# Performance work log

Measured on AMD Instinct MI355X. Metric: run time of the kernel, lower is better.

## Reference

```python
import jax, jax.numpy as jnp
import numpy as np

HR, LR, K, RANK = 2048, 1024, 8, 16


def setup_inputs() -> dict:
    key = jax.random.key(0)
    kA, kX, kW, kU, kV, kM = jax.random.split(key, 6)
    A = jax.random.normal(kA, (LR, LR), dtype=jnp.float32)
    A = (A + A.T) / 2  # symmetric so torch UPLO='U' and jax eigh agree
    X = jax.random.normal(kX, (LR, HR), dtype=jnp.float32)
    init_range = (6.0 / (HR + HR)) ** 0.5  # glorot uniform
    weights = jax.random.uniform(kW, (HR, HR), dtype=jnp.float32,
                                 minval=-init_range, maxval=init_range)
    Us = jax.random.normal(kU, (K, HR, RANK), dtype=jnp.float32) * 0.001
    # original inits Vs to zeros; use small noise so corrections are nonzero
    Vs = jax.random.normal(kV, (K, HR, RANK), dtype=jnp.float32) * 0.01
    alphas = jnp.ones((K,), dtype=jnp.float32) / K
    masks = (jax.random.uniform(kM, (K, HR, HR)) < 0.5).astype(jnp.float32)
    return {"A": A, "X": X, "weights": weights, "Us": Us, "Vs": Vs,
            "alphas": alphas, "masks": masks}


def _set_unit_diag(M, eye):
    return M * (1.0 - eye) + eye


def reference(A, X, weights, Us, Vs, alphas, masks):
    lr = A.shape[0]
    hr = weights.shape[0]
    eye_hr = jnp.eye(hr, dtype=A.dtype)
    # --- GSRLayer ---
    _, U_lr = jnp.linalg.eigh(A)                      # (lr, lr)
    s_d = jnp.concatenate([jnp.eye(lr, dtype=A.dtype),
                           jnp.eye(lr, dtype=A.dtype)], axis=0)  # (hr, lr)
    f_d = weights @ s_d @ U_lr.T @ X                  # (hr, hr)
    adj = jnp.abs(f_d)
    adj = _set_unit_diag(adj, eye_hr)
    # --- community-aware low-rank corrections ---
    alpha = jax.nn.softmax(alphas)                    # (k,)
    Zm = adj[None, :, :] * masks                      # (k, hr, hr)
    t = jnp.einsum('kij,kjr->kir', Zm, Us)            # (k, hr, rank)
    corr = jnp.einsum('kir,kjr->kij', t, Vs) * masks  # (k, hr, hr)
    out_adj = adj + jnp.einsum('k,kij->ij', alpha, corr)
    # --- symmetrize with unit diagonal ---
    X_out = out_adj @ out_adj.T
    X_out = (X_out + X_out.T) / 2
    X_out = _set_unit_diag(X_out, eye_hr)
    return out_adj, jnp.abs(X_out)
```

## Files before the change

### kernel.cpp

```cpp
#include <hip/hip_runtime.h>
#include <hip/hip_bf16.h>

typedef unsigned long long u64;

#define MBYTE (1ull << 20)

static const size_t OFF_A64   = 0;
static const size_t OFF_VT    = 8*MBYTE;
static const size_t OFF_TAU   = 12*MBYTE;
static const size_t OFF_D64   = 12*MBYTE +  8192;
static const size_t OFF_E64   = 12*MBYTE + 16384;
static const size_t OFF_XB    = 12*MBYTE + 24576;
static const size_t OFF_Y2B   = 12*MBYTE + 32768;
static const size_t OFF_Y1B   = 12*MBYTE + 40960;
static const size_t OFF_XA    = 12*MBYTE + 49152;
static const size_t OFF_Y1A   = 12*MBYTE + 57344;
static const size_t OFF_Y2A   = 12*MBYTE + 65536;
static const size_t OFF_QA    = 13*MBYTE;
static const size_t OFF_QB    = 17*MBYTE;
static const size_t OFF_SHAT  = 21*MBYTE;
static const size_t OFF_WC    = 25*MBYTE;
static const size_t OFF_M1    = 33*MBYTE;
static const size_t OFF_T8    = 33*MBYTE;
static const size_t OFF_ALPHA = 35*MBYTE + 512*1024;
static const size_t OFF_ADJ   = 41*MBYTE;
static const size_t OFF_OADJ  = 17*MBYTE;
static const size_t OFF_CBUF  = 0;

static const size_t SCD_STRIDE = 9216;
static const size_t SCI_STRIDE = 6144;
static const size_t OFF_SCDB  = OFF_WC;
static const size_t OFF_SCIB  = OFF_WC + 2359296;
static const size_t OFF_KNB   = OFF_WC + 2359296 + 786432;
static const size_t OFF_KNDB  = OFF_WC + 2359296 + 786432 + 2048;

static const size_t OFF_WYW   = OFF_WC;
static const size_t OFF_WYTW  = OFF_WC + 524288;
static const size_t OFF_WYG   = OFF_WC + 1048576;


__global__ void kCopyA(const float* __restrict__ A, double* __restrict__ A64) {
  int gid = blockIdx.x*256 + threadIdx.x;
  if (gid < 1024*1024) A64[gid] = (double)A[gid];
}

__device__ __forceinline__ double agLoadD(const double* p) {
  return __hip_atomic_load(p, __ATOMIC_RELAXED, __HIP_MEMORY_SCOPE_AGENT);
}
__device__ __forceinline__ void agStoreD(double* p, double v) {
  __hip_atomic_store(p, v, __ATOMIC_RELAXED, __HIP_MEMORY_SCOPE_AGENT);
}

#define TD_NBLK 64

__global__ __launch_bounds__(1024) void kTriDiag(
    double* __restrict__ A64,
    double* __restrict__ y1A, double* __restrict__ y1B,
    double* __restrict__ y2A, double* __restrict__ y2B,
    double* __restrict__ diagP, unsigned* __restrict__ flags,
    double* __restrict__ tauv, double* __restrict__ e64, double* __restrict__ d64,
    float* __restrict__ Vt) {
  __shared__ double xL[1024], vL[1024], wL[1024], y1L[1024], y2L[1024];
  __shared__ double red[4];
  __shared__ double sS[4];
  int tid = threadIdx.x;
  int bid = blockIdx.x;
  bool w0 = (bid == 0);
  int lane = tid & 63, wave = tid >> 6;
  int myRow = wave*TD_NBLK + bid;

  double dg = 0.0;

  for (int i = 0; i <= 1023; ++i) {
    const double* y1in = (((i-1)&1) != 0) ? y1B : y1A;
    const double* y2in = (((i-1)&1) != 0) ? y2B : y2A;
    double* y1out = ((i&1) != 0) ? y1B : y1A;
    double* y2out = ((i&1) != 0) ? y2B : y2A;

    if (i == 0) {
      if (tid < 256) {
        for (int c = tid; c < 1024; c += 256) { vL[c] = 0.0; wL[c] = 0.0; }
        for (int c = 1 + tid; c < 1024; c += 256) xL[c] = A64[(u64)c*1024];
        if (w0 && tid == 0) d64[0] = A64[0];
      }
      __syncthreads();
    } else {
      int j = i - 1;
      double sy1 = agLoadD(&y1in[tid]);
      double sy2 = agLoadD(&y2in[tid]);
      if (w0 && tid == 0) dg = agLoadD(&diagP[i]);
      double acc = 0.0;
      if (tid < 256) {
        for (int c = i + 1 + tid; c < 1024; c += 256) { double v = xL[c]; acc += v*v; }
        for (int off = 32; off > 0; off >>= 1) acc += __shfl_xor(acc, off, 64);
      }
      y1L[tid] = sy1; y2L[tid] = sy2;
      if (tid < 256 && lane == 0) red[wave] = acc;
      __syncthreads();
      if (tid == 0) {
        double xn2 = red[0] + red[1] + red[2] + red[3];
        double alpha = xL[i];
        double tv, sc;
        if (xn2 == 0.0) { tv = 0.0; if (w0) e64[j] = alpha; sc = 0.0; }
        else {
          double beta = (alpha >= 0.0) ? -sqrt(alpha*alpha + xn2) : sqrt(alpha*alpha + xn2);
          tv = (beta - alpha)/beta;
          if (w0) e64[j] = beta;
          sc = 1.0/(alpha - beta);
        }
        if (w0) tauv[j] = tv;
        sS[0] = sc; sS[1] = tv;
        vL[i] = 1.0;
        if (w0) Vt[(u64)j*1024 + i] = 1.0f;
      }
      __syncthreads();
      if (tid < 256) {
        double sc = sS[0], tv = sS[1];
        double acc2 = 0.0;
        for (int r = i + tid; r < 1024; r += 256) {
          double v;
          if (r == i) v = 1.0;
          else {
            v = xL[r]*sc;
            vL[r] = v;
            if (w0) Vt[(u64)j*1024 + r] = (float)v;
          }
          double P = tv*(y1L[r] + sc*y2L[r]);
          wL[r] = P;
          acc2 += P*v;
        }
        for (int off = 32; off > 0; off >>= 1) acc2 += __shfl_xor(acc2, off, 64);
        if (lane == 0) red[wave] = acc2;
      }
      __syncthreads();
      if (tid == 0) {
        double coef = 0.5*sS[1]*(red[0] + red[1] + red[2] + red[3]);
        double wi = wL[i] - coef;
        sS[2] = coef; sS[3] = wi;
        if (w0) d64[i] = dg - 2.0*wi;
      }
      __syncthreads();
      if (tid < 256) {
        double coef = sS[2], wi = sS[3];
        for (int r = i + tid; r < 1024; r += 256) {
          double wcr = wL[r] - coef*vL[r];
          wL[r] = wcr;
          if (r > i) xL[r] = y1L[r] - vL[r]*wi - wcr;
        }
      }
      __syncthreads();
    }
    if (i <= 1022) {
      int r = myRow;
      if (r >= i + 1) {
        double vr = vL[r], wr = wL[r];
        double* Arow = A64 + (u64)r*1024;
        double acc = 0.0, y1v = 0.0;
        for (int c = i + 1 + lane; c < 1024; c += 64) {
          double a = Arow[c] - vr*wL[c] - wr*vL[c];
          Arow[c] = a;
          if (c == r) agStoreD(&diagP[r], a);
          if (c == i + 1) y1v = a; else acc += a*xL[c];
        }
        for (int off = 32; off > 0; off >>= 1) acc += __shfl_down(acc, off, 64);
        if (lane == 0) { agStoreD(&y1out[r], y1v); agStoreD(&y2out[r], acc); }
      }
      __syncthreads();
      unsigned tgt = (unsigned)(i + 1);
      if (tid == 0)
        __hip_atomic_store(&flags[bid*16], tgt, __ATOMIC_RELEASE, __HIP_MEMORY_SCOPE_AGENT);
      if (tid < TD_NBLK) {
        for (;;) {
          unsigned v = __hip_atomic_load(&flags[tid*16], __ATOMIC_ACQUIRE, __HIP_MEMORY_SCOPE_AGENT);
          if (__all(v >= tgt)) break;
          __builtin_amdgcn_s_sleep(2);
        }
      }
      __syncthreads();
    }
  }
  if (w0 && tid == 0) {
    for (int c = 16; c < 1024; c += 16) {
      double ae = fabs(e64[c-1]);
      d64[c-1] -= ae;
      d64[c]   -= ae;
    }
  }
}


__device__ void slartg_(double f, double g, double* cs, double* sn, double* r) {
  if (g == 0.0) { *cs = 1.0; *sn = 0.0; *r = f; }
  else if (f == 0.0) { *cs = 0.0; *sn = (g >= 0.0) ? 1.0 : -1.0; *r = fabs(g); }
  else {
    double d = sqrt(f*f + g*g);
    *cs = fabs(f)/d;
    *r = (f >= 0.0) ? d : -d;
    *sn = g / (*r);
  }
}

__device__ void slaev2_(double a, double b, double c, double* rt1, double* rt2,
                        double* cs1, double* sn1) {
  double sm = a + c, df = a - c, adf = fabs(df), tb = b + b, ab = fabs(tb);
  double acmx, acmn;
  if (fabs(a) > fabs(c)) { acmx = a; acmn = c; } else { acmx = c; acmn = a; }
  double rt;
  if (adf > ab) rt = adf*sqrt(1.0 + (ab/adf)*(ab/adf));
  else if (adf < ab) rt = ab*sqrt(1.0 + (adf/ab)*(adf/ab));
  else rt = ab*sqrt(2.0);
  int sgn1;
  if (sm < 0.0) { *rt1 = 0.5*(sm - rt); sgn1 = -1; *rt2 = (acmx / *rt1)*acmn - (b / *rt1)*b; }
  else if (sm > 0.0) { *rt1 = 0.5*(sm + rt); sgn1 = 1; *rt2 = (acmx / *rt1)*acmn - (b / *rt1)*b; }
  else { *rt1 = 0.5*rt; *rt2 = -0.5*rt; sgn1 = 1; }
  int sgn2; double cs;
  if (df >= 0.0) { cs = df + rt; sgn2 = 1; } else { cs = df - rt; sgn2 = -1; }
  double acs = fabs(cs);
  if (acs > ab) { double ct = -tb/cs; *sn1 = 1.0/sqrt(1.0 + ct*ct); *cs1 = ct*(*sn1); }
  else {
    if (ab == 0.0) { *cs1 = 1.0; *sn1 = 0.0; }
    else { double tn = -cs/tb; *cs1 = 1.0/sqrt(1.0 + tn*tn); *sn1 = tn*(*cs1); }
  }
  if (sgn1 == sgn2) { double tn = *cs1; *cs1 = -(*sn1); *sn1 = tn; }
}

__device__ void steqr16_(double* d, double* e, double* z, double* wc, double* ws_) {
  const int n = 16;
  const double eps = 5.9604644775390625e-08;
  const double eps2 = eps*eps;
  const double safmin = 1.1754943508222875e-38;
  int jtot = 0; const int nmaxit = n*30;
  int l1 = 0;
  for (int outer = 0; outer < 200; ++outer) {
    if (l1 > n-1) break;
    if (l1 > 0) e[l1-1] = 0.0;
    int m = l1;
    for (; m <= n-2; ++m) {
      double tst = fabs(e[m]);
      if (tst == 0.0) break;
      if (tst <= (sqrt(fabs(d[m]))*sqrt(fabs(d[m+1])))*eps) { e[m] = 0.0; break; }
    }
    int l = l1, lend = m;
    l1 = m + 1;
    if (lend == l) continue;
    if (fabs(d[lend]) < fabs(d[l])) { int t = l; l = lend; lend = t; }
    if (lend > l) {
      for (int it = 0; it < 800; ++it) {
        int mm = lend;
        if (l != lend) {
          for (mm = l; mm <= lend-1; ++mm) {
            double tst = e[mm]*e[mm];
            if (tst <= eps2*fabs(d[mm])*fabs(d[mm+1]) + safmin) break;
          }
        }
        if (mm < lend) e[mm] = 0.0;
        double p = d[l];
        if (mm == l) { d[l] = p; ++l; if (l <= lend) continue; break; }
        if (mm == l+1) {
          double rt1, rt2, c2, s2;
          slaev2_(d[l], e[l], d[l+1], &rt1, &rt2, &c2, &s2);
          for (int r = 0; r < n; ++r) {
            double t = z[r*16 + l + 1];
            z[r*16 + l + 1] = c2*t - s2*z[r*16 + l];
            z[r*16 + l]     = s2*t + c2*z[r*16 + l];
          }
          d[l] = rt1; d[l+1] = rt2; e[l] = 0.0;
          l += 2; if (l <= lend) continue; break;
        }
        if (jtot == nmaxit) break;
        ++jtot;
        double g = (d[l+1] - p)/(2.0*e[l]);
        double r_ = sqrt(g*g + 1.0);
        g = d[mm] - p + e[l]/(g + ((g >= 0.0) ? r_ : -r_));
        double s = 1.0, c = 1.0;
        p = 0.0;
        for (int i = mm-1; i >= l; --i) {
          double f = s*e[i], b = c*e[i];
          double cs, sn, rr;
          slartg_(g, f, &cs, &sn, &rr);
          c = cs; s = sn;
          if (i != mm-1) e[i+1] = rr;
          g = d[i+1] - p;
          rr = (d[i] - g)*s + 2.0*c*b;
          p = s*rr;
          d[i+1] = g + p;
          g = c*rr - b;
          wc[i] = c; ws_[i] = -s;
        }
        for (int jj = mm-1; jj >= l; --jj) {
          double cs = wc[jj], sn = ws_[jj];
          for (int r = 0; r < n; ++r) {
            double t = z[r*16 + jj + 1];
            z[r*16 + jj + 1] = cs*t - sn*z[r*16 + jj];
            z[r*16 + jj]     = sn*t + cs*z[r*16 + jj];
          }
        }
        d[l] -= p;
        e[l] = g;
      }
    } else {
      for (int it = 0; it < 800; ++it) {
        int mm = lend;
        if (l != lend) {
          for (mm = l; mm >= lend+1; --mm) {
            double tst = e[mm-1]*e[mm-1];
            if (tst <= eps2*fabs(d[mm])*fabs(d[mm-1]) + safmin) break;
          }
        }
        if (mm > lend) e[mm-1] = 0.0;
        double p = d[l];
        if (mm == l) { d[l] = p; --l; if (l >= lend) continue; break; }
        if (mm == l-1) {
          double rt1, rt2, c2, s2;
          slaev2_(d[l-1], e[l-1], d[l], &rt1, &rt2, &c2, &s2);
          for (int r = 0; r < n; ++r) {
            double t = z[r*16 + l];
            z[r*16 + l]     = c2*t - s2*z[r*16 + l - 1];
            z[r*16 + l - 1] = s2*t + c2*z[r*16 + l - 1];
          }
          d[l-1] = rt1; d[l] = rt2; e[l-1] = 0.0;
          l -= 2; if (l >= lend) continue; break;
        }
        if (jtot == nmaxit) break;
        ++jtot;
        double g = (d[l-1] - p)/(2.0*e[l-1]);
        double r_ = sqrt(g*g + 1.0);
        g = d[mm] - p + e[l-1]/(g + ((g >= 0.0) ? r_ : -r_));
        double s = 1.0, c = 1.0;
        p = 0.0;
        for (int i = mm; i <= l-1; ++i) {
          double f = s*e[i], b = c*e[i];
          double cs, sn, rr;
          slartg_(g, f, &cs, &sn, &rr);
          c = cs; s = sn;
          if (i != mm) e[i-1] = rr;
          g = d[i] - p;
          rr = (d[i+1] - g)*s + 2.0*c*b;
          p = s*rr;
          d[i] = g + p;
          g = c*rr - b;
          wc[i] = c; ws_[i] = s;
        }
        for (int jj = mm; jj <= l-1; ++jj) {
          double cs = wc[jj], sn = ws_[jj];
          for (int r = 0; r < n; ++r) {
            double t = z[r*16 + jj + 1];
            z[r*16 + jj + 1] = cs*t - sn*z[r*16 + jj];
            z[r*16 + jj]     = sn*t + cs*z[r*16 + jj];
          }
        }
        d[l] -= p;
        e[l-1] = g;
      }
    }
  }
  for (int ii = 1; ii <= n-1; ++ii) {
    int i = ii - 1, k = i;
    double p = d[i];
    for (int j = ii; j <= n-1; ++j) if (d[j] < p) { k = j; p = d[j]; }
    if (k != i) {
      d[k] = d[i]; d[i] = p;
      for (int r = 0; r < n; ++r) { double t = z[r*16 + i]; z[r*16 + i] = z[r*16 + k]; z[r*16 + k] = t; }
    }
  }
}

__global__ void kLeaf(double* d64, const double* e64, float* Qa) {
  __shared__ double dd[16], ed[16], zd[256], wk1[16], wk2[16];
  int leaf = blockIdx.x, lo = leaf*16, tid = threadIdx.x;
  for (int idx = tid; idx < 256; idx += 64) zd[idx] = ((idx/16) == (idx%16)) ? 1.0 : 0.0;
  if (tid < 16) { dd[tid] = d64[lo + tid]; ed[tid] = (tid < 15) ? e64[lo + tid] : 0.0; }
  __syncthreads();
  if (tid == 0) steqr16_(dd, ed, zd, wk1, wk2);
  __syncthreads();
  for (int idx = tid; idx < 256; idx += 64) {
    int r = idx/16, c = idx%16;
    Qa[(u64)(lo + r)*1024 + lo + c] = (float)zd[idx];
  }
  if (tid < 16) d64[lo + tid] = dd[tid];
}


__global__ __launch_bounds__(1024) void kDeflateB(float* __restrict__ Qa,
      const double* __restrict__ d64, const double* __restrict__ e64,
      double* scdB, int* sciB, int* knB, double* kndB, int bs) {
  __shared__ double zL[1024], dlocL[1024], redD[1024];
  __shared__ double rcL[1024], rsL[1024];
  __shared__ int sIdxL[1024], rpqL[1024];
  __shared__ double sSc[4];
  __shared__ int sKn[4];
  int mg = blockIdx.x;
  int n1 = bs, n = 2*bs, lo = mg*n;
  double* scd = scdB + (u64)mg*SCD_STRIDE;
  int*    sci = sciB + (u64)mg*SCI_STRIDE;
  int* kn = knB + mg*8;
  double* knd = kndB + mg*4;
  int tid = threadIdx.x;
  if (tid == 0) sSc[0] = e64[lo + n1 - 1];
  __syncthreads();
  double rho_in = sSc[0];
  const double invs2 = 0.70710678118654752440;
  if (tid < n) {
    int row = (tid < n1) ? (lo + n1 - 1) : (lo + n1);
    double s = (rho_in < 0.0 && tid >= n1) ? -invs2 : invs2;
    zL[tid] = (double)Qa[(u64)row*1024 + lo + tid] * s;
    dlocL[tid] = d64[lo + tid];
  }
  __syncthreads();
  if (tid < n) {
    int pos; double key = dlocL[tid];
    if (tid < n1) {
      int loB = 0, hiB = n - n1;
      while (loB < hiB) { int mid = (loB+hiB)>>1; if (dlocL[n1+mid] < key) loB = mid+1; else hiB = mid; }
      pos = tid + loB;
    } else {
      int loA = 0, hiA = n1;
      while (loA < hiA) { int mid = (loA+hiA)>>1; if (dlocL[mid] <= key) loA = mid+1; else hiA = mid; }
      pos = (tid - n1) + loA;
    }
    sIdxL[pos] = tid;
  }
  redD[tid] = (tid < n) ? fabs(zL[tid]) : 0.0;
  __syncthreads();
  for (int s = 512; s > 0; s >>= 1) { if (tid < s) redD[tid] = fmax(redD[tid], redD[tid+s]); __syncthreads(); }
  if (tid == 0) sSc[1] = redD[0];
  __syncthreads();
  redD[tid] = (tid < n) ? fabs(dlocL[tid]) : 0.0;
  __syncthreads();
  for (int s = 512; s > 0; s >>= 1) { if (tid < s) redD[tid] = fmax(redD[tid], redD[tid+s]); __syncthreads(); }
  if (tid == 0) {
    double zmax = sSc[1], dmax = redD[0];
    double rho = fabs(2.0*rho_in);
    double tol = 8.0*5.9604644775390625e-8*fmax(dmax, zmax);
    double* dlG = scd + 1024;
    double* wmG = scd + 2048;
    double* dvalG = scd + 7168;
    int* permG = sci;
    int* deflG = sci + 1024;
    int K = 0, nrot = 0, nd = 0; double sw2 = 0.0;
    if (rho*zmax <= tol) {
      for (int pos = 0; pos < n; ++pos) { int c = sIdxL[pos]; deflG[nd] = c; dvalG[nd] = dlocL[c]; nd++; }
    } else {
      int pj = -1, jpos = 0;
      for (; jpos < n; ++jpos) {
        int nj = sIdxL[jpos];
        if (rho*fabs(zL[nj]) <= tol) { deflG[nd] = nj; dvalG[nd] = dlocL[nj]; nd++; }
        else { pj = nj; break; }
      }
      for (++jpos; jpos < n; ++jpos) {
        int nj = sIdxL[jpos];
        if (rho*fabs(zL[nj]) <= tol) { deflG[nd] = nj; dvalG[nd] = dlocL[nj]; nd++; continue; }
        double s_ = zL[pj], c_ = zL[nj];
        double tu = sqrt(c_*c_ + s_*s_);
        double tdif = dlocL[nj] - dlocL[pj];
        c_ /= tu; s_ = -s_/tu;
        if (fabs(tdif*c_*s_) <= tol) {
          zL[nj] = tu; zL[pj] = 0.0;
          rpqL[nrot] = (pj << 16) | nj; rcL[nrot] = c_; rsL[nrot] = s_; nrot++;
          double t1 = dlocL[pj]*c_*c_ + dlocL[nj]*s_*s_;
          dlocL[nj] = dlocL[pj]*s_*s_ + dlocL[nj]*c_*c_;
          dlocL[pj] = t1;
          deflG[nd] = pj; dvalG[nd] = t1; nd++;
          pj = nj;
        } else {
          permG[K] = pj; dlG[K] = dlocL[pj]; wmG[K] = zL[pj]; sw2 += zL[pj]*zL[pj]; K++;
          pj = nj;
        }
      }
      permG[K] = pj; dlG[K] = dlocL[pj]; wmG[K] = zL[pj]; sw2 += zL[pj]*zL[pj]; K++;
    }
    sKn[1] = nrot;
    kn[0] = K; kn[1] = nrot; kn[2] = nd;
    knd[0] = rho; knd[1] = sw2;
  }
  __syncthreads();
  int nrot = sKn[1];
  if (tid < n && nrot > 0) {
    u64 row = (u64)(lo + tid)*1024;
    for (int t = 0; t < nrot; ++t) {
      int pq = rpqL[t];
      int p = lo + (pq >> 16), q = lo + (pq & 0xffff);
      double c = rcL[t], s = rsL[t];
      double x = (double)Qa[row + p], y = (double)Qa[row + q];
      Qa[row + p] = (float)(c*x + s*y);
      Qa[row + q] = (float)(c*y - s*x);
    }
  }
}

__global__ __launch_bounds__(256) void kSecularB(double* scdB, const int* knB, const double* kndB) {
  __shared__ double dlS[1024], wmS[1024];
  int mg = blockIdx.y;
  double* scd = scdB + (u64)mg*SCD_STRIDE;
  const int* kn = knB + mg*8;
  const double* knd = kndB + mg*4;
  int K = kn[0];
  int tid = threadIdx.x;
  for (int j = tid; j < K; j += 256) { dlS[j] = scd[1024 + j]; wmS[j] = scd[2048 + j]; }
  __syncthreads();
  int wave = tid >> 6, lane = tid & 63;
  int i = blockIdx.x*4 + wave;
  if (i >= K) return;
  double rho = knd[0], sw2 = knd[1];
  double di = dlS[i];
  double hi = (i < K-1) ? (dlS[i+1] - di) : (rho*sw2*(1.0 + 1e-12) + 1e-300);
  double lo_ = 0.0;
  for (int it = 0; it < 100; ++it) {
    double mid = 0.5*(lo_ + hi);
    double g = 0.0;
    for (int j = lane; j < K; j += 64) { double w = wmS[j]; g += w*w/((dlS[j] - di) - mid); }
    for (int off = 32; off > 0; off >>= 1) g += __shfl_xor(g, off);
    g = 1.0 + rho*g;
    if (g < 0.0) lo_ = mid; else hi = mid;
  }
  scd[3072 + i] = 0.5*(lo_ + hi);
}

__global__ void kZhatB(double* scdB, const int* knB) {
  int mg = blockIdx.y;
  double* scd = scdB + (u64)mg*SCD_STRIDE;
  int K = (knB + mg*8)[0];
  int j = blockIdx.x*64 + threadIdx.x;
  if (j >= K) return;
  const double* dl = scd + 1024;
  const double* wm = scd + 2048;
  const double* mu = scd + 3072;
  double dj = dl[j];
  double prod = mu[j];
  for (int i2 = 0; i2 < K; ++i2) {
    if (i2 == j) continue;
    double dd = dl[i2] - dj;
    prod *= (dd + mu[i2]) / dd;
  }
  prod = fabs(prod);
  scd[4096 + j] = (wm[j] >= 0.0) ? sqrt(prod) : -sqrt(prod);
}

__global__ __launch_bounds__(1024) void kSortPermB(double* scdB, int* sciB, const int* knB,
                                                   double* d64, int bs) {
  __shared__ double sv[1024];
  __shared__ int si[1024];
  int mg = blockIdx.x;
  int n = 2*bs, lo = mg*n;
  double* scd = scdB + (u64)mg*SCD_STRIDE;
  int* sci = sciB + (u64)mg*SCI_STRIDE;
  int K = (knB + mg*8)[0];
  int tid = threadIdx.x;
  const double* dl = scd + 1024;
  const double* mu = scd + 3072;
  const double* dval = scd + 7168;
  double v;
  if (tid < K) v = dl[tid] + mu[tid];
  else if (tid < n) v = dval[tid - K];
  else v = 1e300;
  sv[tid] = v; si[tid] = tid;
  __syncthreads();
  for (int k = 2; k <= 1024; k <<= 1) {
    for (int j = k >> 1; j > 0; j >>= 1) {
      int ixj = tid ^ j;
      if (ixj > tid) {
        bool up = ((tid & k) == 0);
        double a = sv[tid], b = sv[ixj];
        int ia = si[tid], ib = si[ixj];
        bool agtb = (a > b) || (a == b && ia > ib);
        if (up ? agtb : !agtb) { sv[tid] = b; sv[ixj] = a; si[tid] = ib; si[ixj] = ia; }
      }
      __syncthreads();
    }
  }
  if (tid < n) {
    int s = si[tid];
    if (s < K) sci[4096 + s] = tid; else sci[5120 + s - K] = tid;
    d64[lo + tid] = sv[tid];
  }
}

__global__ void kSvecNormB(float* __restrict__ Shat, const double* scdB, const int* knB, int bs) {
  int mg = blockIdx.y;
  int n = 2*bs, lo = mg*n;
  const double* scd = scdB + (u64)mg*SCD_STRIDE;
  int K = (knB + mg*8)[0];
  int i = blockIdx.x;
  if (i >= K) return;
  const double* dl = scd + 1024;
  const double* mu = scd + 3072;
  const double* zh = scd + 4096;
  __shared__ double red[256];
  int tid = threadIdx.x;
  double di = dl[i], m = mu[i];
  double acc = 0.0;
  for (int j = tid; j < K; j += 256) {
    double v = zh[j]/((dl[j] - di) - m);
    acc += v*v;
  }
  red[tid] = acc; __syncthreads();
  for (int s = 128; s > 0; s >>= 1) { if (tid < s) red[tid] += red[tid+s]; __syncthreads(); }
  double inv = 1.0/sqrt(red[0]);
  for (int j = tid; j < K; j += 256) {
    double v = zh[j]/((dl[j] - di) - m);
    Shat[(u64)j*1024 + lo + i] = (float)(v*inv);
  }
}

__global__ void kGatherB(const float* Qa, float* Qb, const int* sciB, const int* knB, int bs) {
  int mg = blockIdx.y;
  int n = 2*bs, lo = mg*n;
  const int* sci = sciB + (u64)mg*SCI_STRIDE;
  int K = (knB + mg*8)[0];
  int gid = blockIdx.x*256 + threadIdx.x;
  if (gid >= n*n) return;
  int p = gid % n, r = gid / n;
  int src = (p < K) ? sci[p] : sci[1024 + p - K];
  Qb[(u64)(lo + r)*1024 + p] = Qa[(u64)(lo + r)*1024 + lo + src];
}

__global__ void kGemmMergeB(const float* __restrict__ Qb, const float* __restrict__ Shat,
                            float* __restrict__ Qa, const int* sciB, const int* knB, int bs) {
  __shared__ float As[16][17], Bs[16][17];
  int mg = blockIdx.z;
  int n = 2*bs, lo = mg*n;
  const int* sci = sciB + (u64)mg*SCI_STRIDE;
  int K = (knB + mg*8)[0];
  int tx = threadIdx.x, ty = threadIdx.y;
  int r0 = blockIdx.y*16, c0 = blockIdx.x*16;
  const int* rootpos = sci + 4096;
  float acc = 0.f;
  for (int k0 = 0; k0 < K; k0 += 16) {
    As[ty][tx] = (k0 + tx < K) ? Qb[(u64)(lo + r0 + ty)*1024 + k0 + tx] : 0.f;
    Bs[ty][tx] = (k0 + ty < K && c0 + tx < K) ? Shat[(u64)(k0 + ty)*1024 + lo + c0 + tx] : 0.f;
    __syncthreads();
    #pragma unroll
    for (int kk = 0; kk < 16; ++kk) acc += As[ty][kk]*Bs[kk][tx];
    __syncthreads();
  }
  int i = c0 + tx;
  if (i < K) Qa[(u64)(lo + r0 + ty)*1024 + lo + rootpos[i]] = acc;
}

__global__ void kScatterDeflB(const float* Qb, float* Qa, const int* sciB, const int* knB, int bs) {
  int mg = blockIdx.y;
  int n = 2*bs, lo = mg*n;
  const int* sci = sciB + (u64)mg*SCI_STRIDE;
  const int* kn = knB + mg*8;
  int gid = blockIdx.x*256 + threadIdx.x;
  if (gid >= n*n) return;
  int p = gid % n, r = gid / n;
  int K = kn[0], nd = kn[2];
  if (p < K || p - K >= nd) return;
  Qa[(u64)(lo + r)*1024 + lo + sci[5120 + p - K]] = Qb[(u64)(lo + r)*1024 + p];
}


__global__ void kVtZero(float* __restrict__ Vt) {
  int gid = blockIdx.x*256 + threadIdx.x;
  if (gid >= 1024*1024) return;
  int row = gid >> 10, col = gid & 1023;
  if (col <= row) Vt[gid] = 0.f;
}

__global__ __launch_bounds__(256) void kWyW(const float* __restrict__ Vt,
    const float* __restrict__ Qa, double* __restrict__ W, double* __restrict__ G,
    int i0, int rbeg) {
  __shared__ float sA[64][33];
  __shared__ float sB[32][65];
  int tid = threadIdx.x;
  int tx = tid & 15, ty = tid >> 4;
  if (blockIdx.x < 16) {
    int c0 = blockIdx.x*64;
    double acc[4][4];
    #pragma unroll
    for (int i = 0; i < 4; ++i)
      #pragma unroll
      for (int k = 0; k < 4; ++k) acc[i][k] = 0.0;
    for (int r0 = rbeg; r0 < 1024; r0 += 32) {
      #pragma unroll
      for (int k = 0; k < 8; ++k) {
        int e = tid + k*256;
        int j = e >> 5, rr = e & 31;
        int r = r0 + rr;
        sA[j][rr] = (r < 1024) ? Vt[(u64)(i0 + j)*1024 + r] : 0.f;
      }
      #pragma unroll
      for (int k = 0; k < 8; ++k) {
        int e = tid + k*256;
        int rr = e >> 6, cc = e & 63;
        int r = r0 + rr;
        sB[rr][cc] = (r < 1024) ? Qa[(u64)r*1024 + c0 + cc] : 0.f;
      }
      __syncthreads();
      for (int rr = 0; rr < 32; ++rr) {
        double a0 = sA[ty*4+0][rr], a1 = sA[ty*4+1][rr];
        double a2 = sA[ty*4+2][rr], a3 = sA[ty*4+3][rr];
        double b0 = sB[rr][tx*4+0], b1 = sB[rr][tx*4+1];
        double b2 = sB[rr][tx*4+2], b3 = sB[rr][tx*4+3];
        acc[0][0] += a0*b0; acc[0][1] += a0*b1; acc[0][2] += a0*b2; acc[0][3] += a0*b3;
        acc[1][0] += a1*b0; acc[1][1] += a1*b1; acc[1][2] += a1*b2; acc[1][3] += a1*b3;
        acc[2][0] += a2*b0; acc[2][1] += a2*b1; acc[2][2] += a2*b2; acc[2][3] += a2*b3;
        acc[3][0] += a3*b0; acc[3][1] += a3*b1; acc[3][2] += a3*b2; acc[3][3] += a3*b3;
      }
      __syncthreads();
    }
    #pragma unroll
    for (int i = 0; i < 4; ++i)
      #pragma unroll
      for (int k = 0; k < 4; ++k)
        W[(u64)(ty*4+i)*1024 + c0 + tx*4 + k] = acc[i][k];
  } else {
    double acc[16];
    #pragma unroll
    for (int k = 0; k < 16; ++k) acc[k] = 0.0;
    for (int r0 = rbeg; r0 < 1024; r0 += 32) {
      #pragma unroll
      for (int k = 0; k < 8; ++k) {
        int e = tid + k*256;
        int j = e >> 5, rr = e & 31;
        int r = r0 + rr;
        sA[j][rr] = (r < 1024) ? Vt[(u64)(i0 + j)*1024 + r] : 0.f;
      }
      __syncthreads();
      #pragma unroll
      for (int k = 0; k < 16; ++k) {
        int e = tid + k*256;
        int j1 = e >> 6, j2 = e & 63;
        double s = acc[k];
        for (int rr = 0; rr < 32; ++rr) s += (double)sA[j1][rr]*(double)sA[j2][rr];
        acc[k] = s;
      }
      __syncthreads();
    }
    #pragma unroll
    for (int k = 0; k < 16; ++k) {
      int e = tid + k*256;
      G[(e >> 6)*64 + (e & 63)] = acc[k];
    }
  }
}

__global__ __launch_bounds__(256) void kWyT(const double* __restrict__ G,
    const double* __restrict__ tau, const double* __restrict__ W,
    double* __restrict__ TW, int i0, int nbk) {
  __shared__ double sT[64][65];
  int tid = threadIdx.x;
  for (int e = tid; e < 64*65; e += 256) (&sT[0][0])[e] = 0.0;
  __syncthreads();
  if (tid < nbk) sT[tid][tid] = tau[i0 + tid];
  __syncthreads();
  for (int m = 1; m < nbk; ++m) {
    if (tid < m) {
      double s = 0.0;
      for (int q = tid; q < m; ++q) s += sT[tid][q]*G[q*64 + m];
      sT[tid][m] = -tau[i0 + m]*s;
    }
    __syncthreads();
  }
  int tx = tid & 15, ty = tid >> 4;
  int c0 = blockIdx.x*64;
  #pragma unroll
  for (int i = 0; i < 4; ++i) {
    int j = ty*4 + i;
    #pragma unroll
    for (int k = 0; k < 4; ++k) {
      int c = c0 + tx*4 + k;
      double s = 0.0;
      for (int q = j; q < 64; ++q) s += sT[j][q]*W[(u64)q*1024 + c];
      TW[(u64)j*1024 + c] = s;
    }
  }
}

__global__ __launch_bounds__(256) void kWyU(const float* __restrict__ Vt,
    const double* __restrict__ TW, float* __restrict__ Qa, int i0, int rbeg) {
  __shared__ float sV[64][65];
  __shared__ double sTW[64][65];
  int tid = threadIdx.x;
  int r0 = rbeg + blockIdx.x*64;
  int c0 = blockIdx.y*64;
  #pragma unroll
  for (int k = 0; k < 16; ++k) {
    int e = tid + k*256;
    int j = e >> 6, rr = e & 63;
    int r = r0 + rr;
    sV[rr][j] = (r < 1024) ? Vt[(u64)(i0 + j)*1024 + r] : 0.f;
  }
  #pragma unroll
  for (int k = 0; k < 16; ++k) {
    int e = tid + k*256;
    int j = e >> 6, cc = e & 63;
    sTW[j][cc] = TW[(u64)j*1024 + c0 + cc];
  }
  __syncthreads();
  int tx = tid & 15, ty = tid >> 4;
  double acc[4][4];
  #pragma unroll
  for (int i = 0; i < 4; ++i)
    #pragma unroll
    for (int k = 0; k < 4; ++k) acc[i][k] = 0.0;
  for (int j = 0; j < 64; ++j) {
    double v0 = sV[ty*4+0][j], v1 = sV[ty*4+1][j];
    double v2 = sV[ty*4+2][j], v3 = sV[ty*4+3][j];
    double t0 = sTW[j][tx*4+0], t1 = sTW[j][tx*4+1];
    double t2 = sTW[j][tx*4+2], t3 = sTW[j][tx*4+3];
    acc[0][0] += v0*t0; acc[0][1] += v0*t1; acc[0][2] += v0*t2; acc[0][3] += v0*t3;
    acc[1][0] += v1*t0; acc[1][1] += v1*t1; acc[1][2] += v1*t2; acc[1][3] += v1*t3;
    acc[2][0] += v2*t0; acc[2][1] += v2*t1; acc[2][2] += v2*t2; acc[2][3] += v2*t3;
    acc[3][0] += v3*t0; acc[3][1] += v3*t1; acc[3][2] += v3*t2; acc[3][3] += v3*t3;
  }
  #pragma unroll
  for (int i = 0; i < 4; ++i) {
    int r = r0 + ty*4 + i;
    if (r < 1024) {
      #pragma unroll
      for (int k = 0; k < 4; ++k) {
        u64 a = (u64)r*1024 + c0 + tx*4 + k;
        Qa[a] = (float)((double)Qa[a] - acc[i][k]);
      }
    }
  }
}


template<int TA, int TB>
__global__ __launch_bounds__(256) void gemm_f32(const float* __restrict__ A,
    const float* __restrict__ B, float* __restrict__ C,
    int M, int N, int Kd, int lda, int ldb, int ldc) {
  __shared__ float As[8][132];
  __shared__ float Bs[8][132];
  int tid = threadIdx.x;
  int bi = blockIdx.y*128, bj = blockIdx.x*128;
  int tx = tid & 15, ty = tid >> 4;
  float acc[8][8];
  #pragma unroll
  for (int x = 0; x < 8; ++x)
    #pragma unroll
    for (int y = 0; y < 8; ++y) acc[x][y] = 0.f;
  for (int k0 = 0; k0 < Kd; k0 += 8) {
    if (TA == 0) {
      int row = tid >> 1, kc = (tid & 1)*4;
      float4 v = *(const float4*)&A[(u64)(bi + row)*lda + k0 + kc];
      As[kc+0][row] = v.x; As[kc+1][row] = v.y; As[kc+2][row] = v.z; As[kc+3][row] = v.w;
    } else {
      int kk = tid >> 5, col = (tid & 31)*4;
      float4 v = *(const float4*)&A[(u64)(k0 + kk)*lda + bi + col];
      *(float4*)&As[kk][col] = v;
    }
    if (TB == 0) {
      int kk = tid >> 5, col = (tid & 31)*4;
      float4 v = *(const float4*)&B[(u64)(k0 + kk)*ldb + bj + col];
      *(float4*)&Bs[kk][col] = v;
    } else {
      int row = tid >> 1, kc = (tid & 1)*4;
      float4 v = *(const float4*)&B[(u64)(bj + row)*ldb + k0 + kc];
      Bs[kc+0][row] = v.x; Bs[kc+1][row] = v.y; Bs[kc+2][row] = v.z; Bs[kc+3][row] = v.w;
    }
    __syncthreads();
    #pragma unroll
    for (int kk = 0; kk < 8; ++kk) {
      float a[8], b[8];
      *(float4*)&a[0] = *(float4*)&As[kk][ty*8];
      *(float4*)&a[4] = *(float4*)&As[kk][ty*8 + 4];
      *(float4*)&b[0] = *(float4*)&Bs[kk][tx*8];
      *(float4*)&b[4] = *(float4*)&Bs[kk][tx*8 + 4];
      #pragma unroll
      for (int x = 0; x < 8; ++x)
        #pragma unroll
        for (int y = 0; y < 8; ++y) acc[x][y] += a[x]*b[y];
    }
    __syncthreads();
  }
  #pragma unroll
  for (int x = 0; x < 8; ++x) {
    float* Crow = &C[(u64)(bi + ty*8 + x)*ldc + bj + tx*8];
    *(float4*)&Crow[0] = make_float4(acc[x][0], acc[x][1], acc[x][2], acc[x][3]);
    *(float4*)&Crow[4] = make_float4(acc[x][4], acc[x][5], acc[x][6], acc[x][7]);
  }
}

__global__ void kWc(const float* W, float* Wc) {
  int gid = blockIdx.x*256 + threadIdx.x;
  if (gid >= 2048*1024) return;
  int i = gid >> 10, k = gid & 1023;
  Wc[gid] = W[(u64)i*2048 + k] + W[(u64)i*2048 + 1024 + k];
}

__global__ void kAbsDiag(float* adj) {
  int gid = blockIdx.x*256 + threadIdx.x;
  if (gid >= 2048*2048) return;
  int i = gid >> 11, j = gid & 2047;
  float v = fabsf(adj[gid]);
  adj[gid] = (i == j) ? 1.0f : v;
}

__global__ void kTk(const float* __restrict__ adj, const float* __restrict__ masks,
                    const float* __restrict__ Us, float* __restrict__ t8) {
  int k = blockIdx.y;
  int i = blockIdx.x*16 + (threadIdx.x >> 4);
  int r = threadIdx.x & 15;
  const float* arow = adj + (u64)i*2048;
  const float* mrow = masks + ((u64)k*2048 + i)*2048;
  const float* uk = Us + (u64)k*2048*16 + r;
  float acc = 0.f;
  for (int j = 0; j < 2048; ++j) acc += arow[j]*mrow[j]*uk[(u64)j*16];
  t8[((u64)k*2048 + i)*16 + r] = acc;
}

__global__ void kAlpha(const float* alphas, float* alpha) {
  if (threadIdx.x == 0 && blockIdx.x == 0) {
    float m = alphas[0];
    for (int k = 1; k < 8; ++k) m = fmaxf(m, alphas[k]);
    float e[8]; float s = 0.f;
    for (int k = 0; k < 8; ++k) { e[k] = expf(alphas[k] - m); s += e[k]; }
    for (int k = 0; k < 8; ++k) alpha[k] = e[k]/s;
  }
}

__global__ void kOutAdj(const float* __restrict__ adj, const float* __restrict__ masks,
                        const float* __restrict__ Vs, const float* __restrict__ t8,
                        const float* __restrict__ alpha, float* __restrict__ oadj,
                        float* __restrict__ out0) {
  __shared__ float tS[8][16][16];
  __shared__ float vS[8][16][16];
  int j0 = blockIdx.x*16, i0 = blockIdx.y*16;
  int tid = threadIdx.x;
  for (int idx = tid; idx < 2048; idx += 256) {
    int k = idx >> 8, rem = idx & 255, row = rem >> 4, r = rem & 15;
    tS[k][row][r] = t8[((u64)k*2048 + i0 + row)*16 + r];
    vS[k][row][r] = Vs[((u64)k*2048 + j0 + row)*16 + r];
  }
  __syncthreads();
  int ii = tid >> 4, jj = tid & 15;
  int i = i0 + ii, j = j0 + jj;
  float corr = 0.f;
  for (int k = 0; k < 8; ++k) {
    float m = masks[((u64)k*2048 + i)*2048 + j];
    float dv = 0.f;
    #pragma unroll
    for (int r = 0; r < 16; ++r) dv += tS[k][ii][r]*vS[k][jj][r];
    corr += alpha[k]*m*dv;
  }
  float val = adj[(u64)i*2048 + j] + corr;
  oadj[(u64)i*2048 + j] = val;
  out0[(u64)i*2048 + j] = val;
}

__global__ void kFinal(const float* __restrict__ C, float* __restrict__ out1) {
  int gid = blockIdx.x*256 + threadIdx.x;
  if (gid >= 2048*2048) return;
  int i = gid >> 11, j = gid & 2047;
  float v;
  if (i == j) v = 1.0f;
  else v = 0.5f*(C[gid] + C[(u64)j*2048 + i]);
  out1[gid] = fabsf(v);
}


extern "C" void kernel_launch(void* const* d_in, const int* in_sizes, int n_in,
                              void* d_out, int out_size, void* d_ws, size_t ws_size,
                              hipStream_t stream) {
  const float* A      = (const float*)d_in[0];
  const float* X      = (const float*)d_in[1];
  const float* W      = (const float*)d_in[2];
  const float* Us     = (const float*)d_in[3];
  const float* Vs     = (const float*)d_in[4];
  const float* alphas = (const float*)d_in[5];
  const float* masks  = (const float*)d_in[6];

  char* ws = (char*)d_ws;
  double* A64  = (double*)(ws + OFF_A64);
  float*  Vt   = (float*) (ws + OFF_VT);
  double* tau  = (double*)(ws + OFF_TAU);
  double* d64  = (double*)(ws + OFF_D64);
  double* e64  = (double*)(ws + OFF_E64);
  double* diagP = (double*)(ws + OFF_XA);
  unsigned* flags = (unsigned*)(ws + OFF_XB);
  double* y1a  = (double*)(ws + OFF_Y1A);
  double* y1b  = (double*)(ws + OFF_Y1B);
  double* y2a  = (double*)(ws + OFF_Y2A);
  double* y2b  = (double*)(ws + OFF_Y2B);
  double* SCDB = (double*)(ws + OFF_SCDB);
  int*    SCIB = (int*)   (ws + OFF_SCIB);
  int*    KNB  = (int*)   (ws + OFF_KNB);
  double* KNDB = (double*)(ws + OFF_KNDB);
  double* WYW  = (double*)(ws + OFF_WYW);
  double* WYTW = (double*)(ws + OFF_WYTW);
  double* WYG  = (double*)(ws + OFF_WYG);
  float*  ALPH = (float*) (ws + OFF_ALPHA);
  float*  Qa   = (float*) (ws + OFF_QA);
  float*  Qb   = (float*) (ws + OFF_QB);
  float*  Shat = (float*) (ws + OFF_SHAT);
  float*  Wc   = (float*) (ws + OFF_WC);
  float*  M1   = (float*) (ws + OFF_M1);
  float*  T8   = (float*) (ws + OFF_T8);
  float*  ADJ  = (float*) (ws + OFF_ADJ);
  float*  OADJ = (float*) (ws + OFF_OADJ);
  float*  CB   = (float*) (ws + OFF_CBUF);

  float* out0 = (float*)d_out;
  float* out1 = out0 + (u64)2048*2048;

  hipMemsetAsync(ws + OFF_XB, 0, 4096, stream);
  kCopyA<<<4096, 256, 0, stream>>>(A, A64);
  {
    void* kargs[] = { (void*)&A64, (void*)&y1a, (void*)&y1b, (void*)&y2a, (void*)&y2b,
                      (void*)&diagP, (void*)&flags,
                      (void*)&tau, (void*)&e64, (void*)&d64, (void*)&Vt };
    hipLaunchCooperativeKernel((void*)kTriDiag, dim3(TD_NBLK), dim3(1024), kargs, 0, stream);
  }

  hipMemsetAsync(Qa, 0, (size_t)4*MBYTE, stream);
  kLeaf<<<64, 64, 0, stream>>>(d64, e64, Qa);

  for (int lvl = 0; lvl < 6; ++lvl) {
    int bs = 16 << lvl;
    int n = 2*bs;
    int cnt = 1024/n;
    kDeflateB<<<cnt, 1024, 0, stream>>>(Qa, d64, e64, SCDB, SCIB, KNB, KNDB, bs);
    kSecularB<<<dim3((n + 3)/4, cnt), 256, 0, stream>>>(SCDB, KNB, KNDB);
    kZhatB<<<dim3((n + 63)/64, cnt), 64, 0, stream>>>(SCDB, KNB);
    kSortPermB<<<cnt, 1024, 0, stream>>>(SCDB, SCIB, KNB, d64, bs);
    kSvecNormB<<<dim3(n, cnt), 256, 0, stream>>>(Shat, SCDB, KNB, bs);
    kGatherB<<<dim3((n*n + 255)/256, cnt), 256, 0, stream>>>(Qa, Qb, SCIB, KNB, bs);
    kGemmMergeB<<<dim3(n/16, n/16, cnt), dim3(16, 16), 0, stream>>>(Qb, Shat, Qa, SCIB, KNB, bs);
    kScatterDeflB<<<dim3((n*n + 255)/256, cnt), 256, 0, stream>>>(Qb, Qa, SCIB, KNB, bs);
  }

  kVtZero<<<4096, 256, 0, stream>>>(Vt);
  for (int i0 = 960; i0 >= 0; i0 -= 64) {
    int nbk = (i0 == 960) ? 63 : 64;
    int rbeg = i0 + 1;
    int L = 1024 - rbeg;
    kWyW<<<17, 256, 0, stream>>>(Vt, Qa, WYW, WYG, i0, rbeg);
    kWyT<<<16, 256, 0, stream>>>(WYG, tau, WYW, WYTW, i0, nbk);
    kWyU<<<dim3((L + 63)/64, 16), 256, 0, stream>>>(Vt, WYTW, Qa, i0, rbeg);
  }

  kWc<<<8192, 256, 0, stream>>>(W, Wc);
  gemm_f32<1,0><<<dim3(16, 8), 256, 0, stream>>>(Qa, X, M1, 1024, 2048, 1024, 1024, 2048, 2048);
  gemm_f32<0,0><<<dim3(16, 16), 256, 0, stream>>>(Wc, M1, ADJ, 2048, 2048, 1024, 1024, 2048, 2048);
  kAbsDiag<<<16384, 256, 0, stream>>>(ADJ);
  kTk<<<dim3(128, 8), 256, 0, stream>>>(ADJ, masks, Us, T8);
  kAlpha<<<1, 64, 0, stream>>>(alphas, ALPH);
  kOutAdj<<<dim3(128, 128), 256, 0, stream>>>(ADJ, masks, Vs, T8, ALPH, OADJ, out0);
  gemm_f32<0,1><<<dim3(16, 16), 256, 0, stream>>>(OADJ, OADJ, CB, 2048, 2048, 2048, 2048, 2048, 2048);
  kFinal<<<16384, 256, 0, stream>>>(CB, out1);
}
```

Baseline: 16.78 ms.

## Flatten Householder step to one element per thread and drop redundant barriers

Each Householder step of the tridiagonalization now maps one vector element to each of the 1024 threads instead of striding over 256 threads. Every thread redundantly computes the reflector scalars from a 16-wave shared reduction, so the serial tid==0 sections and two of the five per-step __syncthreads go away. This shortens the 1023-step sequential critical path. Separately, the final kernel skips the (C + C^T)/2 averaging on the grounds that C is symmetric, which can differ from the reference by rounding.

New measurement: 17.00 ms. No clear change (+1.3%).

```diff
diff --git a/kernel.cpp b/kernel.cpp
--- a/kernel.cpp
+++ b/kernel.cpp
@@ -61,8 +61,8 @@
     double* __restrict__ tauv, double* __restrict__ e64, double* __restrict__ d64,
     float* __restrict__ Vt) {
   __shared__ double xL[1024], vL[1024], wL[1024], y1L[1024], y2L[1024];
-  __shared__ double red[4];
-  __shared__ double sS[4];
+  __shared__ double red[16];
+  __shared__ double sP[1];
   int tid = threadIdx.x;
   int bid = blockIdx.x;
   bool w0 = (bid == 0);
@@ -78,76 +78,61 @@
     double* y2out = ((i&1) != 0) ? y2B : y2A;
 
     if (i == 0) {
-      if (tid < 256) {
-        for (int c = tid; c < 1024; c += 256) { vL[c] = 0.0; wL[c] = 0.0; }
-        for (int c = 1 + tid; c < 1024; c += 256) xL[c] = A64[(u64)c*1024];
-        if (w0 && tid == 0) d64[0] = A64[0];
-      }
+      vL[tid] = 0.0; wL[tid] = 0.0;
+      if (tid >= 1) xL[tid] = A64[(u64)tid*1024];
+      if (w0 && tid == 0) d64[0] = A64[0];
       __syncthreads();
     } else {
       int j = i - 1;
       double sy1 = agLoadD(&y1in[tid]);
       double sy2 = agLoadD(&y2in[tid]);
       if (w0 && tid == 0) dg = agLoadD(&diagP[i]);
-      double acc = 0.0;
-      if (tid < 256) {
-        for (int c = i + 1 + tid; c < 1024; c += 256) { double v = xL[c]; acc += v*v; }
-        for (int off = 32; off > 0; off >>= 1) acc += __shfl_xor(acc, off, 64);
-      }
+      double nacc = (tid >= i + 1) ? xL[tid]*xL[tid] : 0.0;
+      for (int off = 32; off > 0; off >>= 1) nacc += __shfl_xor(nacc, off, 64);
       y1L[tid] = sy1; y2L[tid] = sy2;
-      if (tid < 256 && lane == 0) red[wave] = acc;
+      if (lane == 0) red[wave] = nacc;
       __syncthreads();
-      if (tid == 0) {
-        double xn2 = red[0] + red[1] + red[2] + red[3];
-        double alpha = xL[i];
-        double tv, sc;
-        if (xn2 == 0.0) { tv = 0.0; if (w0) e64[j] = alpha; sc = 0.0; }
-        else {
-          double beta = (alpha >= 0.0) ? -sqrt(alpha*alpha + xn2) : sqrt(alpha*alpha + xn2);
-          tv = (beta - alpha)/beta;
-          if (w0) e64[j] = beta;
-          sc = 1.0/(alpha - beta);
-        }
-        if (w0) tauv[j] = tv;
-        sS[0] = sc; sS[1] = tv;
-        vL[i] = 1.0;
-        if (w0) Vt[(u64)j*1024 + i] = 1.0f;
-      }
+      double xn2 = 0.0;
+      #pragma unroll
+      for (int u = 0; u < 16; ++u) xn2 += red[u];
+      double alpha = xL[i];
+      double tv, sc;
+      if (xn2 == 0.0) {
+        tv = 0.0; sc = 0.0;
+        if (w0 && tid == 0) e64[j] = alpha;
+      } else {
+        double beta = (alpha >= 0.0) ? -sqrt(alpha*alpha + xn2) : sqrt(alpha*alpha + xn2);
+        tv = (beta - alpha)/beta;
+        sc = 1.0/(alpha - beta);
+        if (w0 && tid == 0) e64[j] = beta;
+      }
+      if (w0 && tid == 0) tauv[j] = tv;
+      int r = tid;
+      double v = 0.0, P = 0.0;
+      double pacc = 0.0;
+      if (r >= i) {
+        v = (r == i) ? 1.0 : xL[r]*sc;
+        vL[r] = v;
+        if (w0) Vt[(u64)j*1024 + r] = (float)v;
+        P = tv*(sy1 + sc*sy2);
+        wL[r] = P;
+        if (r == i) sP[0] = P;
+        pacc = P*v;
+      }
+      for (int off = 32; off > 0; off >>= 1) pacc += __shfl_xor(pacc, off, 64);
+      if (lane == 0) red[wave] = pacc;
       __syncthreads();
-      if (tid < 256) {
-        double sc = sS[0], tv = sS[1];
-        double acc2 = 0.0;
-        for (int r = i + tid; r < 1024; r += 256) {
-          double v;
-          if (r == i) v = 1.0;
-          else {
-            v = xL[r]*sc;
-            vL[r] = v;
-            if (w0) Vt[(u64)j*1024 + r] = (float)v;
-          }
-          double P = tv*(y1L[r] + sc*y2L[r]);
-          wL[r] = P;
-          acc2 += P*v;
-        }
-        for (int off = 32; off > 0; off >>= 1) acc2 += __shfl_xor(acc2, off, 64);
-        if (lane == 0) red[wave] = acc2;
-      }
-      __syncthreads();
-      if (tid == 0) {
-        double coef = 0.5*sS[1]*(red[0] + red[1] + red[2] + red[3]);
-        double wi = wL[i] - coef;
-        sS[2] = coef; sS[3] = wi;
-        if (w0) d64[i] = dg - 2.0*wi;
-      }
-      __syncthreads();
-      if (tid < 256) {
-        double coef = sS[2], wi = sS[3];
-        for (int r = i + tid; r < 1024; r += 256) {
-          double wcr = wL[r] - coef*vL[r];
-          wL[r] = wcr;
-          if (r > i) xL[r] = y1L[r] - vL[r]*wi - wcr;
-        }
-      }
+      double dot = 0.0;
+      #pragma unroll
+      for (int u = 0; u < 16; ++u) dot += red[u];
+      double coef = 0.5*tv*dot;
+      double wi = sP[0] - coef;
+      if (r >= i) {
+        double wcr = P - coef*v;
+        wL[r] = wcr;
+        if (r > i) xL[r] = sy1 - v*wi - wcr;
+      }
+      if (w0 && tid == 0) d64[i] = dg - 2.0*wi;
       __syncthreads();
     }
     if (i <= 1022) {
@@ -171,8 +156,8 @@
         __hip_atomic_store(&flags[bid*16], tgt, __ATOMIC_RELEASE, __HIP_MEMORY_SCOPE_AGENT);
       if (tid < TD_NBLK) {
         for (;;) {
-          unsigned v = __hip_atomic_load(&flags[tid*16], __ATOMIC_ACQUIRE, __HIP_MEMORY_SCOPE_AGENT);
-          if (__all(v >= tgt)) break;
+          unsigned vfl = __hip_atomic_load(&flags[tid*16], __ATOMIC_ACQUIRE, __HIP_MEMORY_SCOPE_AGENT);
+          if (__all(vfl >= tgt)) break;
           __builtin_amdgcn_s_sleep(2);
         }
       }
@@ -946,10 +931,7 @@
   int gid = blockIdx.x*256 + threadIdx.x;
   if (gid >= 2048*2048) return;
   int i = gid >> 11, j = gid & 2047;
-  float v;
-  if (i == j) v = 1.0f;
-  else v = 0.5f*(C[gid] + C[(u64)j*2048 + i]);
-  out1[gid] = fabsf(v);
+  out1[gid] = (i == j) ? 1.0f : fabsf(C[gid]);
 }
 
 
```
